# Performance work log

Hardware: AMD Instinct MI355X
Metric: run time of the kernel (lower is better)

The kernel has to match this reference:

```python
import jax, jax.numpy as jnp
import numpy as np

B, S, HID = 2, 2048, 2048
NH, NKV, HD = 16, 4, 128
G = NH // NKV  # kv group size
EPS = 1e-6


def setup_inputs() -> dict:
    key = jax.random.key(0)
    ks = jax.random.split(key, 7)
    w = 0.02
    return {
        "hidden_states": jax.random.normal(ks[0], (B, S, HID), dtype=jnp.float32),
        "position_ids": jnp.broadcast_to(jnp.arange(S, dtype=jnp.int64), (B, S)),
        "Wq": jax.random.normal(ks[1], (2 * NH * HD, HID), dtype=jnp.float32) * w,
        "Wk": jax.random.normal(ks[2], (NKV * HD, HID), dtype=jnp.float32) * w,
        "Wv": jax.random.normal(ks[3], (NKV * HD, HID), dtype=jnp.float32) * w,
        "Wo": jax.random.normal(ks[4], (HID, NH * HD), dtype=jnp.float32) * w,
        "norm_w": jnp.zeros((HID,), dtype=jnp.float32),
    }


def reference(hidden_states, position_ids, Wq, Wk, Wv, Wo, norm_w):
    # RMSNorm (weight parameterized as 1 + w, per source)
    ms = jnp.mean(hidden_states * hidden_states, axis=-1, keepdims=True)
    x = hidden_states * jax.lax.rsqrt(ms + EPS) * (1.0 + norm_w)

    qg = x @ Wq.T                                   # (B,S,2*NH*HD)
    q, gate = jnp.split(qg, 2, axis=-1)
    q = q.reshape(B, S, NH, HD).transpose(0, 2, 1, 3)       # (B,NH,S,HD)
    gate = gate.reshape(B, S, NH, HD).transpose(0, 2, 1, 3)
    k = (x @ Wk.T).reshape(B, S, NKV, HD).transpose(0, 2, 1, 3)  # (B,NKV,S,HD)
    v = (x @ Wv.T).reshape(B, S, NKV, HD).transpose(0, 2, 1, 3)

    scale = 1.0 / np.sqrt(HD).astype(np.float32)
    qg4 = q.reshape(B, NKV, G, S, HD)
    attn = jnp.einsum("bkgqd,bkld->bkgql", qg4, k) * scale   # (B,NKV,G,S,S)
    p = jax.nn.softmax(attn, axis=-1)
    o = jnp.einsum("bkgql,bkld->bkgqd", p, v).reshape(B, NH, S, HD)

    o = o * jax.nn.sigmoid(gate)                    # output gate
    o = o.transpose(0, 2, 1, 3).reshape(B, S, NH * HD)
    return o @ Wo.T
```

## Files before the change

kernel.cpp:

```cpp
#include <hip/hip_runtime.h>
#include <math.h>

#define BB    2
#define SS    2048
#define HIDD  2048
#define NHH   16
#define NKVV  4
#define HDD   128
#define MROWS 4096
#define QG_N  4096
#define KV_N  512
#define O_N   2048
#define KDIM  2048
#define EPS_  1e-6f
#define SCALE_ 0.08838834764831845f

typedef __attribute__((ext_vector_type(8))) __bf16 bf16x8;
typedef __attribute__((ext_vector_type(8))) unsigned short u16x8;
typedef __attribute__((ext_vector_type(4))) float f32x4;

__device__ __forceinline__ unsigned short f2bf(float f) {
  return __builtin_bit_cast(unsigned short, (__bf16)f);
}

__global__ __launch_bounds__(256) void f2bf_k(const float* __restrict__ in,
                                              unsigned short* __restrict__ out, int n4) {
  int i = blockIdx.x * 256 + threadIdx.x;
  if (i < n4) {
    float4 v = ((const float4*)in)[i];
    ushort4 u;
    u.x = f2bf(v.x); u.y = f2bf(v.y); u.z = f2bf(v.z); u.w = f2bf(v.w);
    ((ushort4*)out)[i] = u;
  }
}

__global__ __launch_bounds__(256) void rmsnorm_k(const float* __restrict__ h,
                                                 const float* __restrict__ w,
                                                 unsigned short* __restrict__ x) {
  int row = blockIdx.x;
  int t = threadIdx.x;
  const float4* hr = (const float4*)(h + (size_t)row * HIDD);
  const float4* w4 = (const float4*)w;

  float4 v0 = hr[t], v1 = hr[t + 256];
  float ss = v0.x*v0.x + v0.y*v0.y + v0.z*v0.z + v0.w*v0.w
           + v1.x*v1.x + v1.y*v1.y + v1.z*v1.z + v1.w*v1.w;
#pragma unroll
  for (int off = 32; off > 0; off >>= 1) ss += __shfl_down(ss, off, 64);

  __shared__ float part[4];
  __shared__ float rs_sh;
  if ((t & 63) == 0) part[t >> 6] = ss;
  __syncthreads();
  if (t == 0) rs_sh = rsqrtf((part[0]+part[1]+part[2]+part[3]) * (1.0f/HIDD) + EPS_);
  __syncthreads();
  float rs = rs_sh;

  float4 w0 = w4[t], w1 = w4[t + 256];
  ushort4 o0, o1;
  o0.x = f2bf(v0.x * rs * (1.f + w0.x));
  o0.y = f2bf(v0.y * rs * (1.f + w0.y));
  o0.z = f2bf(v0.z * rs * (1.f + w0.z));
  o0.w = f2bf(v0.w * rs * (1.f + w0.w));
  o1.x = f2bf(v1.x * rs * (1.f + w1.x));
  o1.y = f2bf(v1.y * rs * (1.f + w1.y));
  o1.z = f2bf(v1.z * rs * (1.f + w1.z));
  o1.w = f2bf(v1.w * rs * (1.f + w1.w));
  ushort4* xr = (ushort4*)(x + (size_t)row * HIDD);
  xr[t] = o0;
  xr[t + 256] = o1;
}

template <int OBF>
__device__ __forceinline__ void gemm_core(const unsigned short* __restrict__ Ab,
                                          const unsigned short* __restrict__ Bb,
                                          void* __restrict__ Cv,
                                          void* __restrict__ Cv2,
                                          int Ndim, int bm, int bn,
                                          unsigned short* Als, unsigned short* Bls) {
  char* ldsA = (char*)Als;
  char* ldsB = (char*)Bls;

  int t   = threadIdx.x;
  int r15 = t & 15;
  int g   = (t & 63) >> 4;
  int w   = t >> 6;
  int wr  = w >> 1, wc = w & 1;

  f32x4 acc[4][4] = {};

  for (int k0 = 0; k0 < KDIM; k0 += 64) {
    __syncthreads();
#pragma unroll
    for (int it = 0; it < 4; ++it) {
      int f      = it * 256 + t;
      int row    = f >> 3;
      int schunk = (f & 7) ^ (row & 7);
      unsigned ldsbase = (unsigned)((it * 256 + (w << 6)) << 4);
      __builtin_amdgcn_global_load_lds(
          (const unsigned int*)(Ab + ((size_t)(bm + row) << 11) + k0 + schunk * 8),
          (unsigned int*)(ldsA + ldsbase), 16, 0, 0);
      __builtin_amdgcn_global_load_lds(
          (const unsigned int*)(Bb + ((size_t)(bn + row) << 11) + k0 + schunk * 8),
          (unsigned int*)(ldsB + ldsbase), 16, 0, 0);
    }
    __syncthreads();

#pragma unroll
    for (int tt = 0; tt < 2; ++tt) {
      bf16x8 af[4], bfv[4];
#pragma unroll
      for (int mi = 0; mi < 4; ++mi) {
        int row = wr * 64 + mi * 16 + r15;
        af[mi] = *(const bf16x8*)(ldsA + row * 128 + (((4 * tt + g) ^ (row & 7)) << 4));
      }
#pragma unroll
      for (int ni = 0; ni < 4; ++ni) {
        int row = wc * 64 + ni * 16 + r15;
        bfv[ni] = *(const bf16x8*)(ldsB + row * 128 + (((4 * tt + g) ^ (row & 7)) << 4));
      }
      __builtin_amdgcn_s_setprio(1);
#pragma unroll
      for (int mi = 0; mi < 4; ++mi)
#pragma unroll
        for (int ni = 0; ni < 4; ++ni)
          acc[mi][ni] = __builtin_amdgcn_mfma_f32_16x16x32_bf16(af[mi], bfv[ni], acc[mi][ni], 0, 0, 0);
      __builtin_amdgcn_s_setprio(0);
    }
  }

#pragma unroll
  for (int mi = 0; mi < 4; ++mi)
#pragma unroll
    for (int ni = 0; ni < 4; ++ni) {
      int col = bn + wc * 64 + ni * 16 + r15;
#pragma unroll
      for (int r = 0; r < 4; ++r) {
        int rowg = bm + wr * 64 + mi * 16 + g * 4 + r;
        if (OBF == 1)
          ((unsigned short*)Cv)[(size_t)rowg * Ndim + col] = f2bf(acc[mi][ni][r]);
        else if (OBF == 2) {
          if (col < O_N)
            ((unsigned short*)Cv)[(size_t)rowg * O_N + col] = f2bf(acc[mi][ni][r] * SCALE_);
          else
            ((float*)Cv2)[(size_t)rowg * O_N + (col - O_N)] = acc[mi][ni][r];
        } else
          ((float*)Cv)[(size_t)rowg * Ndim + col] = acc[mi][ni][r];
      }
    }
}

template <int OBF>
__global__ __launch_bounds__(256) void gemm_bf16(const unsigned short* __restrict__ Ab,
                                                 const unsigned short* __restrict__ Bb,
                                                 void* __restrict__ Cv,
                                                 int Ndim) {
  __shared__ unsigned short Als[128 * 64];
  __shared__ unsigned short Bls[128 * 64];
  gemm_core<OBF>(Ab, Bb, Cv, nullptr, Ndim, blockIdx.y * 128, blockIdx.x * 128, Als, Bls);
}

__global__ __launch_bounds__(256) void gemm_qg(const unsigned short* __restrict__ Ab,
                                               const unsigned short* __restrict__ Bb,
                                               unsigned short* __restrict__ Cq,
                                               float* __restrict__ Cg) {
  __shared__ unsigned short Als[128 * 64];
  __shared__ unsigned short Bls[128 * 64];
  gemm_core<2>(Ab, Bb, (void*)Cq, (void*)Cg, QG_N, blockIdx.y * 128, blockIdx.x * 128, Als, Bls);
}

__global__ __launch_bounds__(256) void gemm_kv(const unsigned short* __restrict__ Ab,
                                               const unsigned short* __restrict__ Wk,
                                               const unsigned short* __restrict__ Wv,
                                               unsigned short* __restrict__ Ck,
                                               unsigned short* __restrict__ Cva) {
  __shared__ unsigned short Als[128 * 64];
  __shared__ unsigned short Bls[128 * 64];
  int bx = blockIdx.x;
  const unsigned short* Bb = (bx < 4) ? Wk : Wv;
  unsigned short* Cv = (bx < 4) ? Ck : Cva;
  gemm_core<1>(Ab, Bb, (void*)Cv, nullptr, KV_N, blockIdx.y * 128, (bx & 3) * 128, Als, Bls);
}

__global__ __launch_bounds__(256, 2) void attn_mfma(const unsigned short* __restrict__ qb,
                                                    const float* __restrict__ gateb,
                                                    const unsigned short* __restrict__ kb,
                                                    const unsigned short* __restrict__ vb,
                                                    unsigned short* __restrict__ obuf) {
  __shared__ unsigned short Ks[2][64 * 128];
  __shared__ unsigned short Vt[2][64 * 128];
  __shared__ unsigned short Ps[4][32 * 64];
  char* ldsK0 = (char*)Ks;
  char* ldsV0 = (char*)Vt;

  int t = threadIdx.x;
  int l = t & 63, w = t >> 6;
  int c15 = l & 15, g = l >> 4;
  char* ldsP = (char*)(Ps[w]);
  int bid = blockIdx.x;
  int swz = (bid & 7) * 64 + (bid >> 3);
  int qt = swz & 15, h = (swz >> 4) & 15, b = swz >> 8;
  int kh = h >> 2;
  size_t rowQ0 = (size_t)b * SS + (size_t)qt * 128;
  size_t rowKbase = (size_t)b * SS;

  bf16x8 qf[2][4];
#pragma unroll
  for (int qi = 0; qi < 2; ++qi)
#pragma unroll
    for (int ks = 0; ks < 4; ++ks)
      qf[qi][ks] = *(const bf16x8*)(qb + (rowQ0 + w * 32 + qi * 16 + c15) * O_N
                                       + h * HDD + g * 8 + ks * 32);

  f32x4 accO[2][8] = {};
  float mrun[2] = {-INFINITY, -INFINITY};
  float lrun[2] = {0.f, 0.f};
  u16x8 vreg[4];

#define ISSUE_K(bufi, kt_)                                                     \
  {                                                                            \
    size_t rowK0 = rowKbase + (size_t)(kt_) * 64;                              \
    _Pragma("unroll")                                                          \
    for (int it = 0; it < 4; ++it) {                                           \
      int f = it * 256 + t;                                                    \
      int kv = f >> 4;                                                         \
      int schunk = (f & 15) ^ (kv & 7);                                        \
      unsigned ldsbase = (unsigned)((it * 256 + (w << 6)) << 4);               \
      __builtin_amdgcn_global_load_lds(                                        \
          (const unsigned int*)(kb + (rowK0 + kv) * KV_N + kh * HDD + schunk * 8), \
          (unsigned int*)(ldsK0 + (bufi) * 16384 + ldsbase), 16, 0, 0);        \
    }                                                                          \
  }
#define ISSUE_V(kt_)                                                           \
  {                                                                            \
    size_t rowK0 = rowKbase + (size_t)(kt_) * 64;                              \
    _Pragma("unroll")                                                          \
    for (int it = 0; it < 4; ++it) {                                           \
      int f = it * 256 + t;                                                    \
      int kv = f & 63;                                                         \
      int d8 = (f >> 6) * 8;                                                   \
      vreg[it] = *(const u16x8*)(vb + (rowK0 + kv) * KV_N + kh * HDD + d8);    \
    }                                                                          \
  }
#define WRITE_V(bufi)                                                          \
  {                                                                            \
    _Pragma("unroll")                                                          \
    for (int it = 0; it < 4; ++it) {                                           \
      int f = it * 256 + t;                                                    \
      int kv = f & 63;                                                         \
      int d8 = (f >> 6) * 8;                                                   \
      _Pragma("unroll")                                                        \
      for (int i = 0; i < 8; ++i) {                                            \
        int d = d8 + i;                                                        \
        *(unsigned short*)(ldsV0 + (bufi) * 16384 + d * 128 +                  \
                           (((kv >> 3) ^ (d & 7)) << 4) + (kv & 7) * 2) = vreg[it][i]; \
      }                                                                        \
    }                                                                          \
  }

  ISSUE_K(0, 0);
  ISSUE_V(0);
  asm volatile("s_waitcnt vmcnt(0)" ::: "memory");
  WRITE_V(0);
  __syncthreads();

  const int NT = SS / 64;
  for (int kt = 0; kt < NT; ++kt) {
    int cur = kt & 1, nxt = cur ^ 1;
    char* ldsK = ldsK0 + cur * 16384;
    char* ldsV = ldsV0 + cur * 16384;

    if (kt + 1 < NT) {
      ISSUE_K(nxt, kt + 1);
      ISSUE_V(kt + 1);
    }

    f32x4 accS[2][4] = {};
    __builtin_amdgcn_s_setprio(1);
#pragma unroll
    for (int nf = 0; nf < 4; ++nf) {
      int kvr = nf * 16 + c15;
#pragma unroll
      for (int ks = 0; ks < 4; ++ks) {
        bf16x8 kf = *(const bf16x8*)(ldsK + kvr * 256 + ((((g + 4 * ks) ^ (kvr & 7)) << 4)));
#pragma unroll
        for (int qi = 0; qi < 2; ++qi)
          accS[qi][nf] = __builtin_amdgcn_mfma_f32_16x16x32_bf16(kf, qf[qi][ks], accS[qi][nf], 0, 0, 0);
      }
    }
    __builtin_amdgcn_s_setprio(0);

    float mt[2];
#pragma unroll
    for (int qi = 0; qi < 2; ++qi) {
      float m0 = fmaxf(fmaxf(accS[qi][0][0], accS[qi][0][1]), fmaxf(accS[qi][0][2], accS[qi][0][3]));
#pragma unroll
      for (int nf = 1; nf < 4; ++nf)
        m0 = fmaxf(m0, fmaxf(fmaxf(accS[qi][nf][0], accS[qi][nf][1]), fmaxf(accS[qi][nf][2], accS[qi][nf][3])));
      m0 = fmaxf(m0, __shfl_xor(m0, 16, 64));
      m0 = fmaxf(m0, __shfl_xor(m0, 32, 64));
      mt[qi] = m0;
    }

    bool safe = (mt[0] <= mrun[0] + 8.f) && (mt[1] <= mrun[1] + 8.f);
    if (!__all(safe)) {
#pragma unroll
      for (int qi = 0; qi < 2; ++qi) {
        float mnew = fmaxf(mrun[qi], mt[qi]);
        float al = __expf(mrun[qi] - mnew);
        mrun[qi] = mnew;
        lrun[qi] *= al;
        float alr[4];
#pragma unroll
        for (int r = 0; r < 4; ++r) alr[r] = __shfl(al, g * 4 + r, 16);
#pragma unroll
        for (int df = 0; df < 8; ++df)
#pragma unroll
          for (int r = 0; r < 4; ++r) accO[qi][df][r] *= alr[r];
      }
    }

#pragma unroll
    for (int qi = 0; qi < 2; ++qi) {
      float ps = 0.f;
#pragma unroll
      for (int nf = 0; nf < 4; ++nf) {
        float p0 = __expf(accS[qi][nf][0] - mrun[qi]);
        float p1 = __expf(accS[qi][nf][1] - mrun[qi]);
        float p2 = __expf(accS[qi][nf][2] - mrun[qi]);
        float p3 = __expf(accS[qi][nf][3] - mrun[qi]);
        ps += (p0 + p1) + (p2 + p3);
        ushort4 pk;
        pk.x = f2bf(p0); pk.y = f2bf(p1); pk.z = f2bf(p2); pk.w = f2bf(p3);
        int q = qi * 16 + c15;
        *(ushort4*)(ldsP + q * 128 + ((((nf << 2) + g) ^ (q & 15)) << 3)) = pk;
      }
      ps += __shfl_xor(ps, 16, 64);
      ps += __shfl_xor(ps, 32, 64);
      lrun[qi] += ps;
    }
    asm volatile("s_waitcnt lgkmcnt(0)" ::: "memory");

    __builtin_amdgcn_s_setprio(1);
#pragma unroll
    for (int ks2 = 0; ks2 < 2; ++ks2) {
      bf16x8 pf[2];
#pragma unroll
      for (int qi = 0; qi < 2; ++qi) {
        int q = qi * 16 + c15;
        int ch0 = ((ks2 << 3) + (g << 1)) ^ (q & 15);
        int ch1 = ((ks2 << 3) + (g << 1) + 1) ^ (q & 15);
        ushort4 lo = *(const ushort4*)(ldsP + q * 128 + (ch0 << 3));
        ushort4 hi = *(const ushort4*)(ldsP + q * 128 + (ch1 << 3));
        u16x8 p8 = {lo.x, lo.y, lo.z, lo.w, hi.x, hi.y, hi.z, hi.w};
        pf[qi] = __builtin_bit_cast(bf16x8, p8);
      }
#pragma unroll
      for (int df = 0; df < 8; ++df) {
        int d = df * 16 + c15;
        bf16x8 vf = *(const bf16x8*)(ldsV + d * 128 + ((((g + 4 * ks2) ^ (d & 7)) << 4)));
#pragma unroll
        for (int qi = 0; qi < 2; ++qi)
          accO[qi][df] = __builtin_amdgcn_mfma_f32_16x16x32_bf16(pf[qi], vf, accO[qi][df], 0, 0, 0);
      }
    }
    __builtin_amdgcn_s_setprio(0);

    if (kt + 1 < NT) {
      asm volatile("s_waitcnt vmcnt(0)" ::: "memory");
      WRITE_V(nxt);
    }
    __syncthreads();
  }

#pragma unroll
  for (int qi = 0; qi < 2; ++qi) {
    float invL = 1.f / lrun[qi];
    float ivr[4];
#pragma unroll
    for (int r = 0; r < 4; ++r) ivr[r] = __shfl(invL, g * 4 + r, 16);
#pragma unroll
    for (int r = 0; r < 4; ++r) {
      size_t row = rowQ0 + w * 32 + qi * 16 + g * 4 + r;
#pragma unroll
      for (int df = 0; df < 8; ++df) {
        int d = df * 16 + c15;
        float gt = gateb[row * (size_t)O_N + h * HDD + d];
        float sg = 1.f / (1.f + __expf(-gt));
        obuf[row * (size_t)O_N + h * HDD + d] = f2bf(accO[qi][df][r] * ivr[r] * sg);
      }
    }
  }
#undef ISSUE_K
#undef ISSUE_V
#undef WRITE_V
}

extern "C" void kernel_launch(void* const* d_in, const int* in_sizes, int n_in,
                              void* d_out, int out_size, void* d_ws, size_t ws_size,
                              hipStream_t stream) {
  const float* hs = (const float*)d_in[0];
  const float* Wq = (const float*)d_in[2];
  const float* Wk = (const float*)d_in[3];
  const float* Wv = (const float*)d_in[4];
  const float* Wo = (const float*)d_in[5];
  const float* nw = (const float*)d_in[6];
  float* out = (float*)d_out;

  float* gateb = (float*)d_ws;
  unsigned short* qb16 = (unsigned short*)(gateb + (size_t)MROWS * O_N);
  unsigned short* kb16 = qb16 + (size_t)MROWS * O_N;
  unsigned short* vb16 = kb16 + (size_t)MROWS * KV_N;
  unsigned short* xb   = vb16 + (size_t)MROWS * KV_N;
  unsigned short* ob   = xb   + (size_t)MROWS * HIDD;
  unsigned short* wqb  = ob   + (size_t)MROWS * O_N;
  unsigned short* wkb  = wqb  + (size_t)QG_N * KDIM;
  unsigned short* wvb  = wkb  + (size_t)KV_N * KDIM;
  unsigned short* wob  = wvb  + (size_t)KV_N * KDIM;

  f2bf_k<<<(QG_N*KDIM/4 + 255)/256, 256, 0, stream>>>(Wq, wqb, QG_N*KDIM/4);
  f2bf_k<<<(KV_N*KDIM/4 + 255)/256, 256, 0, stream>>>(Wk, wkb, KV_N*KDIM/4);
  f2bf_k<<<(KV_N*KDIM/4 + 255)/256, 256, 0, stream>>>(Wv, wvb, KV_N*KDIM/4);
  f2bf_k<<<(O_N*KDIM/4  + 255)/256, 256, 0, stream>>>(Wo, wob, O_N*KDIM/4);
  rmsnorm_k<<<MROWS, 256, 0, stream>>>(hs, nw, xb);

  gemm_qg<<<dim3(QG_N/128, MROWS/128), 256, 0, stream>>>(xb, wqb, qb16, gateb);
  gemm_kv<<<dim3(8, MROWS/128), 256, 0, stream>>>(xb, wkb, wvb, kb16, vb16);
  attn_mfma<<<dim3(512), 256, 0, stream>>>(qb16, gateb, kb16, vb16, ob);
  gemm_bf16<0><<<dim3(O_N/128, MROWS/128), 256, 0, stream>>>(ob, wob, out, O_N);
}
```

Baseline: 292.3 us.

## Keep softmax probabilities in registers by permuting V's LDS layout

Removes the per-warp LDS staging buffer for the bf16 probability tile. The P values now go straight from the S accumulator registers into the A operand of the PV MFMA. To make the register layout match, V's kv index is permuted when it is written to LDS, so the MFMA reduction order lines up with the S accumulator layout. This removes the LDS writes and reads, the lgkmcnt wait, and 16KB of shared memory per block. It relies on the permutation being exactly right for correctness.

Result: faster. 286.3 us (-2.0%).

```diff
diff --git a/kernel.cpp b/kernel.cpp
--- a/kernel.cpp
+++ b/kernel.cpp
@@ -189,14 +189,12 @@
                                                     unsigned short* __restrict__ obuf) {
   __shared__ unsigned short Ks[2][64 * 128];
   __shared__ unsigned short Vt[2][64 * 128];
-  __shared__ unsigned short Ps[4][32 * 64];
   char* ldsK0 = (char*)Ks;
   char* ldsV0 = (char*)Vt;
 
   int t = threadIdx.x;
   int l = t & 63, w = t >> 6;
   int c15 = l & 15, g = l >> 4;
-  char* ldsP = (char*)(Ps[w]);
   int bid = blockIdx.x;
   int swz = (bid & 7) * 64 + (bid >> 3);
   int qt = swz & 15, h = (swz >> 4) & 15, b = swz >> 8;
@@ -248,12 +246,13 @@
     for (int it = 0; it < 4; ++it) {                                           \
       int f = it * 256 + t;                                                    \
       int kv = f & 63;                                                         \
+      int sig = (kv & 32) + ((kv & 12) << 1) + ((kv & 16) >> 2) + (kv & 3);    \
       int d8 = (f >> 6) * 8;                                                   \
       _Pragma("unroll")                                                        \
       for (int i = 0; i < 8; ++i) {                                            \
         int d = d8 + i;                                                        \
         *(unsigned short*)(ldsV0 + (bufi) * 16384 + d * 128 +                  \
-                           (((kv >> 3) ^ (d & 7)) << 4) + (kv & 7) * 2) = vreg[it][i]; \
+                           (((sig >> 3) ^ (d & 7)) << 4) + (sig & 7) * 2) = vreg[it][i]; \
       }                                                                        \
     }                                                                          \
   }
@@ -320,6 +319,7 @@
       }
     }
 
+    u16x8 pfr[2][2];
 #pragma unroll
     for (int qi = 0; qi < 2; ++qi) {
       float ps = 0.f;
@@ -330,38 +330,27 @@
         float p2 = __expf(accS[qi][nf][2] - mrun[qi]);
         float p3 = __expf(accS[qi][nf][3] - mrun[qi]);
         ps += (p0 + p1) + (p2 + p3);
-        ushort4 pk;
-        pk.x = f2bf(p0); pk.y = f2bf(p1); pk.z = f2bf(p2); pk.w = f2bf(p3);
-        int q = qi * 16 + c15;
-        *(ushort4*)(ldsP + q * 128 + ((((nf << 2) + g) ^ (q & 15)) << 3)) = pk;
+        pfr[qi][nf >> 1][(nf & 1) * 4 + 0] = f2bf(p0);
+        pfr[qi][nf >> 1][(nf & 1) * 4 + 1] = f2bf(p1);
+        pfr[qi][nf >> 1][(nf & 1) * 4 + 2] = f2bf(p2);
+        pfr[qi][nf >> 1][(nf & 1) * 4 + 3] = f2bf(p3);
       }
       ps += __shfl_xor(ps, 16, 64);
       ps += __shfl_xor(ps, 32, 64);
       lrun[qi] += ps;
     }
-    asm volatile("s_waitcnt lgkmcnt(0)" ::: "memory");
 
     __builtin_amdgcn_s_setprio(1);
 #pragma unroll
     for (int ks2 = 0; ks2 < 2; ++ks2) {
-      bf16x8 pf[2];
-#pragma unroll
-      for (int qi = 0; qi < 2; ++qi) {
-        int q = qi * 16 + c15;
-        int ch0 = ((ks2 << 3) + (g << 1)) ^ (q & 15);
-        int ch1 = ((ks2 << 3) + (g << 1) + 1) ^ (q & 15);
-        ushort4 lo = *(const ushort4*)(ldsP + q * 128 + (ch0 << 3));
-        ushort4 hi = *(const ushort4*)(ldsP + q * 128 + (ch1 << 3));
-        u16x8 p8 = {lo.x, lo.y, lo.z, lo.w, hi.x, hi.y, hi.z, hi.w};
-        pf[qi] = __builtin_bit_cast(bf16x8, p8);
-      }
+      bf16x8 pf0 = __builtin_bit_cast(bf16x8, pfr[0][ks2]);
+      bf16x8 pf1 = __builtin_bit_cast(bf16x8, pfr[1][ks2]);
 #pragma unroll
       for (int df = 0; df < 8; ++df) {
         int d = df * 16 + c15;
         bf16x8 vf = *(const bf16x8*)(ldsV + d * 128 + ((((g + 4 * ks2) ^ (d & 7)) << 4)));
-#pragma unroll
-        for (int qi = 0; qi < 2; ++qi)
-          accO[qi][df] = __builtin_amdgcn_mfma_f32_16x16x32_bf16(pf[qi], vf, accO[qi][df], 0, 0, 0);
+        accO[0][df] = __builtin_amdgcn_mfma_f32_16x16x32_bf16(pf0, vf, accO[0][df], 0, 0, 0);
+        accO[1][df] = __builtin_amdgcn_mfma_f32_16x16x32_bf16(pf1, vf, accO[1][df], 0, 0, 0);
       }
     }
     __builtin_amdgcn_s_setprio(0);
```
